# Kernel optimization log

Hardware: AMD Instinct MI355X
Metric: run time of the kernel (lower is better)

## Reference

```python
import jax, jax.numpy as jnp
import numpy as np

B, N, H, D = 16, 512, 8, 128  # batch, nodes, heads, hid_dim (per-head dim == hid_dim)


def setup_inputs() -> dict:
    key = jax.random.key(0)
    ks = jax.random.split(key, 12)
    x = jax.random.normal(ks[0], (B, N, D), dtype=jnp.float32)
    dist = jax.random.normal(ks[1], (B, N, N), dtype=jnp.float32)
    mask = (jax.random.uniform(ks[2], (B, N)) < 0.9).astype(jnp.float32)
    w_std = 0.02
    Wq = jax.random.normal(ks[3], (D, H * D), dtype=jnp.float32) * w_std
    Wk = jax.random.normal(ks[4], (D, H * D), dtype=jnp.float32) * w_std
    Wv = jax.random.normal(ks[5], (D, H * D), dtype=jnp.float32) * w_std
    Wo = jax.random.normal(ks[6], (H * D, D), dtype=jnp.float32) * w_std
    bq = jax.random.normal(ks[7], (H * D,), dtype=jnp.float32) * w_std
    bk = jax.random.normal(ks[8], (H * D,), dtype=jnp.float32) * w_std
    bv = jax.random.normal(ks[9], (H * D,), dtype=jnp.float32) * w_std
    bo = jax.random.normal(ks[10], (D,), dtype=jnp.float32) * w_std
    return {"x": x, "dist": dist, "mask": mask,
            "Wq": Wq, "bq": bq, "Wk": Wk, "bk": bk,
            "Wv": Wv, "bv": bv, "Wo": Wo, "bo": bo}


def reference(x, dist, mask, Wq, bq, Wk, bk, Wv, bv, Wo, bo):
    scale = jnp.asarray(D, x.dtype) ** -0.5
    # projections: [B,N,H*D] -> [B,H,N,D]
    q = (x @ Wq + bq).reshape(B, N, H, D).transpose(0, 2, 1, 3)
    k = (x @ Wk + bk).reshape(B, N, H, D).transpose(0, 2, 1, 3)
    v = (x @ Wv + bv).reshape(B, N, H, D).transpose(0, 2, 1, 3)
    m = mask[:, None, :, None]  # [B,1,N,1]
    q = q * m * scale
    k = k * m
    v = v * m
    a = jnp.einsum('bhnd,bhmd->bhnm', q, k)  # [B,H,N,N]
    a = a + dist[:, None, :, :]  # dist bias broadcast over heads
    amask = (mask[:, :, None] * mask[:, None, :])[:, None, :, :]  # [B,1,N,N]
    a = jnp.where(amask == 0, jnp.asarray(-1e9, a.dtype), a)
    a = jax.nn.softmax(a, axis=-1)
    a = jnp.where(amask == 0, jnp.asarray(0.0, a.dtype), a)
    y = jnp.einsum('bhnm,bhmd->bhnd', a, v)
    y = y.transpose(0, 2, 1, 3).reshape(B, N, H * D)
    y = y @ Wo + bo
    return y * mask[:, :, None]
```

## Files before the change

### kernel.cpp

```cpp
#include <hip/hip_runtime.h>
#include <hip/hip_bf16.h>

#define B_ 16
#define N_ 512
#define H_ 8
#define D_ 128
#define HD_ 1024
#define SCALE_ 0.08838834764831845f

typedef __attribute__((ext_vector_type(8))) short bf16x8;
typedef __attribute__((ext_vector_type(4))) float f32x4;
typedef __attribute__((ext_vector_type(4))) _Float16 f16x4;

__device__ __forceinline__ unsigned short f2bf(float f) {
    union { __hip_bfloat16 h; unsigned short u; } cv;
    cv.h = __float2bfloat16(f);
    return cv.u;
}
__device__ __forceinline__ unsigned short f2h(float f) {
    union { _Float16 h; unsigned short u; } cv;
    cv.h = (_Float16)f;
    return cv.u;
}

__global__ __launch_bounds__(256) void prep_kernel(
    const float* __restrict__ Wq, const float* __restrict__ Wk,
    const float* __restrict__ Wv, const float* __restrict__ Wo,
    unsigned short* __restrict__ wTh, unsigned short* __restrict__ woT)
{
    __shared__ float T[32][33];
    const int tile = blockIdx.x;
    const int t = threadIdx.x;
    if (tile < 384) {
        const int w = tile / 128;
        const int rem = tile % 128;
        const int kt = rem & 3;
        const int ct = rem >> 2;
        const float* W = (w == 0) ? Wq : (w == 1) ? Wk : Wv;
        const int k0 = kt * 32, c0 = ct * 32;
        #pragma unroll
        for (int u = 0; u < 4; u++) {
            int lin = t + 256 * u; int r = lin >> 5, c = lin & 31;
            T[r][c] = W[(size_t)(k0 + r) * 1024 + c0 + c];
        }
        __syncthreads();
        unsigned short* oh = wTh + (size_t)w * 131072;
        #pragma unroll
        for (int u = 0; u < 4; u++) {
            int lin = t + 256 * u; int c = lin >> 5, r = lin & 31;
            oh[(size_t)(c0 + c) * 128 + k0 + r] = f2bf(T[r][c]);
        }
    } else {
        const int rem = tile - 384;
        const int nt = rem & 3;
        const int kt = rem >> 2;
        const int k0 = kt * 32, n0 = nt * 32;
        #pragma unroll
        for (int u = 0; u < 4; u++) {
            int lin = t + 256 * u; int r = lin >> 5, c = lin & 31;
            T[r][c] = Wo[(size_t)(k0 + r) * 128 + n0 + c];
        }
        __syncthreads();
        #pragma unroll
        for (int u = 0; u < 4; u++) {
            int lin = t + 256 * u; int c = lin >> 5, r = lin & 31;
            woT[(size_t)(n0 + c) * 1024 + k0 + r] = f2bf(T[r][c]);
        }
    }
}

__global__ __launch_bounds__(256, 3) void qkv_kernel(
    const float* __restrict__ x, const float* __restrict__ mask,
    const unsigned short* __restrict__ wTh,
    const float* __restrict__ bq, const float* __restrict__ bk,
    const float* __restrict__ bv,
    unsigned short* __restrict__ q, unsigned short* __restrict__ k,
    unsigned short* __restrict__ vT)
{
    const int cb = blockIdx.x % 24;
    const int by = blockIdx.x / 24;
    const int row0 = by * 128, c0 = cb * 128;
    const int which = c0 >> 10, w0 = c0 & 1023;
    const float* bi = (which == 0) ? bq : (which == 1) ? bk : bv;

    __shared__ alignas(16) unsigned short Wh[128][136];
    __shared__ float biS[128];
    __shared__ float mskS[128];

    const int t = threadIdx.x;
    if (t < 128) { biS[t] = bi[w0 + t]; mskS[t] = mask[row0 + t]; }

    const unsigned short* whp = wTh + (size_t)which * 131072 + (size_t)w0 * 128;
    #pragma unroll
    for (int u = 0; u < 8; u++) {
        int lin = t + 256 * u; int c = lin >> 4, k8 = (lin & 15) * 8;
        *(bf16x8*)&Wh[c][k8] = *(const bf16x8*)&whp[(size_t)c * 128 + k8];
    }

    const int wave = t >> 6, lane = t & 63, m16 = lane & 15, g4 = lane >> 4;
    const int rw = row0 + wave * 32;

    bf16x8 ah[2][4];
    #pragma unroll
    for (int mt = 0; mt < 2; mt++)
        #pragma unroll
        for (int kc = 0; kc < 4; kc++) {
            const float* xp = &x[(size_t)(rw + mt * 16 + m16) * 128 + kc * 32 + g4 * 8];
            float4 v0 = *(const float4*)xp;
            float4 v1 = *(const float4*)(xp + 4);
            float vv[8] = {v0.x, v0.y, v0.z, v0.w, v1.x, v1.y, v1.z, v1.w};
            union { bf16x8 v; unsigned short s[8]; } Hh;
            #pragma unroll
            for (int e = 0; e < 8; e++) Hh.s[e] = f2bf(vv[e]);
            ah[mt][kc] = Hh.v;
        }
    __syncthreads();

    const f32x4 zero = {0.f, 0.f, 0.f, 0.f};
    f32x4 acc[2][8];
    #pragma unroll
    for (int mt = 0; mt < 2; mt++)
        #pragma unroll
        for (int nt = 0; nt < 8; nt++) acc[mt][nt] = zero;

    #pragma unroll
    for (int nt = 0; nt < 8; nt++) {
        #pragma unroll
        for (int kc = 0; kc < 4; kc++) {
            bf16x8 bh = *(const bf16x8*)&Wh[nt * 16 + m16][kc * 32 + g4 * 8];
            #pragma unroll
            for (int mt = 0; mt < 2; mt++)
                acc[mt][nt] = __builtin_amdgcn_mfma_f32_16x16x32_bf16(ah[mt][kc], bh, acc[mt][nt], 0, 0, 0);
        }
    }
    __syncthreads();

    const int b = row0 >> 9, h = w0 >> 7;
    const int iseq0 = row0 & 511;
    unsigned short* Tr = &Wh[0][0];

    if (which == 2) {
        #pragma unroll
        for (int mt = 0; mt < 2; mt++)
            #pragma unroll
            for (int nt = 0; nt < 8; nt++)
                #pragma unroll
                for (int r = 0; r < 4; r++) {
                    int rowl = wave * 32 + mt * 16 + g4 * 4 + r;
                    int col = nt * 16 + m16;
                    Tr[col * 136 + rowl] = f2h((acc[mt][nt][r] + biS[col]) * mskS[rowl]);
                }
        __syncthreads();
        unsigned short* vbase = vT + (size_t)(b * 8 + h) * 128 * 512 + iseq0;
        #pragma unroll
        for (int u = 0; u < 8; u++) {
            int lin = t + 256 * u; int dl = lin >> 4, i8 = (lin & 15) * 8;
            *(bf16x8*)&vbase[(size_t)dl * 512 + i8] = *(const bf16x8*)&Tr[dl * 136 + i8];
        }
    } else {
        const float sc = (which == 0) ? SCALE_ : 1.0f;
        #pragma unroll
        for (int mt = 0; mt < 2; mt++)
            #pragma unroll
            for (int nt = 0; nt < 8; nt++)
                #pragma unroll
                for (int r = 0; r < 4; r++) {
                    int rowl = wave * 32 + mt * 16 + g4 * 4 + r;
                    int col = nt * 16 + m16;
                    Tr[rowl * 136 + col] = f2bf((acc[mt][nt][r] + biS[col]) * (mskS[rowl] * sc));
                }
        __syncthreads();
        unsigned short* dst = ((which == 0) ? q : k) +
                              ((size_t)(b * 8 + h) * 512 + iseq0) * 128;
        #pragma unroll
        for (int u = 0; u < 8; u++) {
            int lin = t + 256 * u; int rl = lin >> 4, c8 = (lin & 15) * 8;
            *(bf16x8*)&dst[(size_t)rl * 128 + c8] = *(const bf16x8*)&Tr[rl * 136 + c8];
        }
    }
}

__global__ __launch_bounds__(256, 3) void attn_kernel(
    const unsigned short* __restrict__ q, const unsigned short* __restrict__ k,
    const unsigned short* __restrict__ vT, const float* __restrict__ dist,
    const float* __restrict__ mask, unsigned short* __restrict__ y)
{
    const int xid = blockIdx.x;
    const int bh = (xid & 7) | ((xid >> 6) << 3);
    const int itile = (xid >> 3) & 7;
    const int b = bh >> 3, h = bh & 7;
    const int i0 = itile * 64;

    const unsigned short* qb = q + (size_t)bh * 512 * 128;
    const unsigned short* kb = k + (size_t)bh * 512 * 128;
    const unsigned short* vb = vT + (size_t)bh * 128 * 512;

    __shared__ alignas(16) unsigned short Ks[64][136];
    __shared__ alignas(16) unsigned short Vs[128][76];
    __shared__ alignas(16) float cmS[512];

    const int t = threadIdx.x;
    const int wave = t >> 6, lane = t & 63;
    const int m16 = lane & 15, g4 = lane >> 4;
    const int iw = i0 + wave * 16;

    cmS[t] = (mask[b * 512 + t] == 0.0f) ? -1e9f : 0.0f;
    cmS[256 + t] = (mask[b * 512 + 256 + t] == 0.0f) ? -1e9f : 0.0f;

    bf16x8 aq[4];
    #pragma unroll
    for (int c = 0; c < 4; c++)
        aq[c] = *(const bf16x8*)(qb + (size_t)(iw + m16) * 128 + c * 32 + g4 * 8);

    const int krow = t >> 2, kcol = (t & 3) * 32;
    const int vrow = t >> 1, vcol = (t & 1) * 32;

    const float* dbase = dist + ((size_t)b * 512 + iw) * 512;

    float4 dvA[4];
    {
        bf16x8 kp[4], vp[4];
        #pragma unroll
        for (int u = 0; u < 4; u++) {
            kp[u] = *(const bf16x8*)(kb + (size_t)krow * 128 + kcol + u * 8);
            vp[u] = *(const bf16x8*)(vb + (size_t)vrow * 512 + vcol + u * 8);
        }
        #pragma unroll
        for (int jt = 0; jt < 4; jt++)
            dvA[jt] = *(const float4*)&dbase[(size_t)m16 * 512 + jt * 16 + g4 * 4];
        #pragma unroll
        for (int u = 0; u < 4; u++) {
            *(bf16x8*)&Ks[krow][kcol + u * 8] = kp[u];
            union { bf16x8 v8; ushort4 h4[2]; } cv; cv.v8 = vp[u];
            *(ushort4*)&Vs[vrow][vcol + u * 8] = cv.h4[0];
            *(ushort4*)&Vs[vrow][vcol + u * 8 + 4] = cv.h4[1];
        }
    }
    __syncthreads();

    const f32x4 zero = {0.f, 0.f, 0.f, 0.f};
    float rm = -3.0e38f, rl = 0.f;
    f32x4 Ot[8] = {zero, zero, zero, zero, zero, zero, zero, zero};

    for (int c = 0; c < 8; c++) {
        const int j0 = c * 64;
        bf16x8 kp[4], vp[4];
        float4 dvB[4];
        if (c < 7) {
            const int j0n = j0 + 64;
            #pragma unroll
            for (int u = 0; u < 4; u++) {
                kp[u] = *(const bf16x8*)(kb + (size_t)(j0n + krow) * 128 + kcol + u * 8);
                vp[u] = *(const bf16x8*)(vb + (size_t)vrow * 512 + j0n + vcol + u * 8);
            }
            #pragma unroll
            for (int jt = 0; jt < 4; jt++)
                dvB[jt] = *(const float4*)&dbase[(size_t)m16 * 512 + j0n + jt * 16 + g4 * 4];
        }

        f32x4 s[4];
        #pragma unroll
        for (int jt = 0; jt < 4; jt++) {
            float4 cm4 = *(const float4*)&cmS[j0 + jt * 16 + g4 * 4];
            f32x4 a = {dvA[jt].x + cm4.x, dvA[jt].y + cm4.y,
                       dvA[jt].z + cm4.z, dvA[jt].w + cm4.w};
            #pragma unroll
            for (int cc = 0; cc < 4; cc++) {
                bf16x8 kf = *(const bf16x8*)&Ks[jt * 16 + m16][cc * 32 + g4 * 8];
                a = __builtin_amdgcn_mfma_f32_16x16x32_bf16(kf, aq[cc], a, 0, 0, 0);
            }
            s[jt] = a;
        }

        float cm = -3.0e38f;
        #pragma unroll
        for (int jt = 0; jt < 4; jt++)
            #pragma unroll
            for (int r = 0; r < 4; r++) cm = fmaxf(cm, s[jt][r]);
        cm = fmaxf(cm, __shfl_xor(cm, 16));
        cm = fmaxf(cm, __shfl_xor(cm, 32));

        float nm = fmaxf(rm, cm);
        float alpha = __expf(rm - nm);
        rm = nm;
        rl *= alpha;

        f16x4 pa[4];
        float ps = 0.f;
        #pragma unroll
        for (int jt = 0; jt < 4; jt++) {
            #pragma unroll
            for (int r = 0; r < 4; r++) {
                float p = __expf(s[jt][r] - rm);
                ps += p;
                pa[jt][r] = (_Float16)p;
            }
        }
        ps += __shfl_xor(ps, 16);
        ps += __shfl_xor(ps, 32);
        rl += ps;

        float a4[4];
        #pragma unroll
        for (int r = 0; r < 4; r++) a4[r] = __shfl(alpha, g4 * 4 + r);
        #pragma unroll
        for (int dt = 0; dt < 8; dt++)
            #pragma unroll
            for (int r = 0; r < 4; r++) Ot[dt][r] *= a4[r];

        #pragma unroll
        for (int jt = 0; jt < 4; jt++)
            #pragma unroll
            for (int dt = 0; dt < 8; dt++) {
                f16x4 vf = *(const f16x4*)&Vs[dt * 16 + m16][jt * 16 + g4 * 4];
                Ot[dt] = __builtin_amdgcn_mfma_f32_16x16x16f16(pa[jt], vf, Ot[dt], 0, 0, 0);
            }

        if (c < 7) {
            __syncthreads();
            #pragma unroll
            for (int u = 0; u < 4; u++) {
                *(bf16x8*)&Ks[krow][kcol + u * 8] = kp[u];
                union { bf16x8 v8; ushort4 h4[2]; } cv; cv.v8 = vp[u];
                *(ushort4*)&Vs[vrow][vcol + u * 8] = cv.h4[0];
                *(ushort4*)&Vs[vrow][vcol + u * 8 + 4] = cv.h4[1];
            }
            #pragma unroll
            for (int jt = 0; jt < 4; jt++) dvA[jt] = dvB[jt];
            __syncthreads();
        }
    }

    __syncthreads();
    float rs = (rl > 0.f) ? 1.0f / rl : 0.f;
    float rs4[4];
    #pragma unroll
    for (int r = 0; r < 4; r++) rs4[r] = __shfl(rs, g4 * 4 + r);
    #pragma unroll
    for (int dt = 0; dt < 8; dt++)
        #pragma unroll
        for (int r = 0; r < 4; r++)
            Ks[wave * 16 + g4 * 4 + r][dt * 16 + m16] = f2bf(Ot[dt][r] * rs4[r]);
    #pragma unroll
    for (int u = 0; u < 4; u++) {
        int lin = lane + 64 * u;
        int row = lin >> 4, seg = lin & 15;
        *(bf16x8*)&y[((size_t)(b * 512) + iw + row) * 1024 + h * 128 + seg * 8] =
            *(const bf16x8*)&Ks[wave * 16 + row][seg * 8];
    }
}

__global__ __launch_bounds__(256, 2) void oproj_kernel(
    const unsigned short* __restrict__ Y, const unsigned short* __restrict__ woT,
    const float* __restrict__ bo, const float* __restrict__ mask,
    float* __restrict__ out)
{
    const int row0 = blockIdx.x * 16;
    __shared__ alignas(16) unsigned short Ys[16][136];
    __shared__ alignas(16) unsigned short Ws[128][136];
    __shared__ float boS[128];
    __shared__ float mskS[16];

    const int t = threadIdx.x;
    if (t < 128) boS[t] = bo[t];
    if (t < 16) mskS[t] = mask[row0 + t];

    const int wave = t >> 6, lane = t & 63;
    const int m16 = lane & 15, g4 = lane >> 4;
    const int n0 = wave * 32;

    const int yr = t >> 4, yk = (t & 15) * 8;
    const int wn = t >> 4, wk = (t & 15) * 8;

    const f32x4 zero = {0.f, 0.f, 0.f, 0.f};
    f32x4 acc[2] = {zero, zero};

    bf16x8 yp, wp[8];
    yp = *(const bf16x8*)&Y[(size_t)(row0 + yr) * 1024 + yk];
    #pragma unroll
    for (int u = 0; u < 8; u++)
        wp[u] = *(const bf16x8*)&woT[(size_t)(wn + u * 16) * 1024 + wk];

    for (int c = 0; c < 8; c++) {
        __syncthreads();
        *(bf16x8*)&Ys[yr][yk] = yp;
        #pragma unroll
        for (int u = 0; u < 8; u++) *(bf16x8*)&Ws[wn + u * 16][wk] = wp[u];
        __syncthreads();
        if (c < 7) {
            const int kc0 = (c + 1) * 128;
            yp = *(const bf16x8*)&Y[(size_t)(row0 + yr) * 1024 + kc0 + yk];
            #pragma unroll
            for (int u = 0; u < 8; u++)
                wp[u] = *(const bf16x8*)&woT[(size_t)(wn + u * 16) * 1024 + kc0 + wk];
        }
        #pragma unroll
        for (int kc = 0; kc < 4; kc++) {
            bf16x8 a = *(const bf16x8*)&Ys[m16][kc * 32 + g4 * 8];
            #pragma unroll
            for (int nt = 0; nt < 2; nt++) {
                bf16x8 bb = *(const bf16x8*)&Ws[n0 + nt * 16 + m16][kc * 32 + g4 * 8];
                acc[nt] = __builtin_amdgcn_mfma_f32_16x16x32_bf16(a, bb, acc[nt], 0, 0, 0);
            }
        }
    }
    __syncthreads();

    float* Ot = (float*)&Ws[0][0];
    #pragma unroll
    for (int nt = 0; nt < 2; nt++)
        #pragma unroll
        for (int r = 0; r < 4; r++) {
            int rowl = g4 * 4 + r;
            int col = n0 + nt * 16 + m16;
            Ot[rowl * 132 + col] = (acc[nt][r] + boS[col]) * mskS[rowl];
        }
    __syncthreads();
    #pragma unroll
    for (int u = 0; u < 2; u++) {
        int lin = t + 256 * u; int r = lin >> 5, c4 = lin & 31;
        *(float4*)&out[(size_t)(row0 + r) * 128 + c4 * 4] =
            *(const float4*)&Ot[r * 132 + c4 * 4];
    }
}

extern "C" void kernel_launch(void* const* d_in, const int* in_sizes, int n_in,
                              void* d_out, int out_size, void* d_ws, size_t ws_size,
                              hipStream_t stream) {
    const float* x    = (const float*)d_in[0];
    const float* dist = (const float*)d_in[1];
    const float* mask = (const float*)d_in[2];
    const float* Wq   = (const float*)d_in[3];
    const float* bq   = (const float*)d_in[4];
    const float* Wk   = (const float*)d_in[5];
    const float* bk   = (const float*)d_in[6];
    const float* Wv   = (const float*)d_in[7];
    const float* bv   = (const float*)d_in[8];
    const float* Wo   = (const float*)d_in[9];
    const float* bo   = (const float*)d_in[10];
    float* out = (float*)d_out;

    const size_t per = (size_t)B_ * H_ * N_ * D_;
    unsigned short* qb  = (unsigned short*)d_ws;
    unsigned short* kb  = qb + per;
    unsigned short* vb  = kb + per;
    unsigned short* yb  = vb + per;
    unsigned short* wTh = yb + per;
    unsigned short* woT = wTh + 3 * 131072;

    prep_kernel<<<512, 256, 0, stream>>>(Wq, Wk, Wv, Wo, wTh, woT);
    qkv_kernel<<<1536, 256, 0, stream>>>(x, mask, wTh, bq, bk, bv, qb, kb, vb);
    attn_kernel<<<1024, 256, 0, stream>>>(qb, kb, vb, dist, mask, yb);
    oproj_kernel<<<512, 256, 0, stream>>>(yb, woT, bo, mask, out);
}
```

Baseline: 161.6 us.

## Double-buffer K/V tiles in LDS with two-deep register prefetch in attention

The attention kernel now keeps two shared-memory buffers for the K and V tiles. It holds register prefetches for the next two 64-key chunks and unrolls the loop in pairs through a macro. Each chunk writes the following tile into the alternate buffer while computing on the current one, so it needs one barrier per chunk instead of two. This hides global-load latency and cuts synchronisation, at the cost of about twice the LDS and more registers. Launch bounds drop from 3 to 2 blocks per CU to fit that.

Result: no change. 162.8 us (+0.7%).

```diff
diff --git a/kernel.cpp b/kernel.cpp
--- a/kernel.cpp
+++ b/kernel.cpp
@@ -180,7 +180,91 @@
     }
 }
 
-__global__ __launch_bounds__(256, 3) void attn_kernel(
+#define ATTN_CHUNK(J0, BSEL, kpC, vpC, dvC, kpO, vpO, DO_LOAD, DO_WRITE, DO_BAR) \
+  {                                                                           \
+    const int j0_ = (J0);                                                     \
+                                     \
+    f32x4 s_[4];                                                              \
+    _Pragma("unroll")                                                         \
+    for (int jt = 0; jt < 4; jt++) {                                          \
+      float4 cm4 = *(const float4*)&cmS[j0_ + jt * 16 + g4 * 4];              \
+      f32x4 a = {dvC[jt].x + cm4.x, dvC[jt].y + cm4.y,                        \
+                 dvC[jt].z + cm4.z, dvC[jt].w + cm4.w};                       \
+      _Pragma("unroll")                                                       \
+      for (int cc = 0; cc < 4; cc++) {                                        \
+        bf16x8 kf = *(const bf16x8*)&Ks[BSEL][jt * 16 + m16][cc * 32 + g4 * 8];\
+        a = __builtin_amdgcn_mfma_f32_16x16x32_bf16(kf, aq[cc], a, 0, 0, 0);  \
+      }                                                                       \
+      s_[jt] = a;                                                             \
+    }                                                                         \
+               \
+    if (DO_LOAD) {                                                            \
+      const int j0n_ = j0_ + 128;                                             \
+      _Pragma("unroll")                                                       \
+      for (int u = 0; u < 4; u++) {                                           \
+        kpC[u] = *(const bf16x8*)(kb + (size_t)(j0n_ + krow) * 128 + kcol + u * 8); \
+        vpC[u] = *(const bf16x8*)(vb + (size_t)vrow * 512 + j0n_ + vcol + u * 8);   \
+      }                                                                       \
+      _Pragma("unroll")                                                       \
+      for (int jt = 0; jt < 4; jt++)                                          \
+        dvC[jt] = *(const float4*)&dbase[(size_t)m16 * 512 + j0n_ + jt * 16 + g4 * 4]; \
+    }                                                                         \
+                                                                 \
+    float cmax_ = -3.0e38f;                                                   \
+    _Pragma("unroll")                                                         \
+    for (int jt = 0; jt < 4; jt++)                                            \
+      _Pragma("unroll")                                                       \
+      for (int r = 0; r < 4; r++) cmax_ = fmaxf(cmax_, s_[jt][r]);            \
+    cmax_ = fmaxf(cmax_, __shfl_xor(cmax_, 16));                              \
+    cmax_ = fmaxf(cmax_, __shfl_xor(cmax_, 32));                              \
+    float nm_ = fmaxf(rm, cmax_);                                             \
+    float alpha_ = __expf(rm - nm_);                                          \
+    rm = nm_;                                                                 \
+    rl *= alpha_;                                                             \
+    f16x4 pa_[4];                                                             \
+    float ps_ = 0.f;                                                          \
+    _Pragma("unroll")                                                         \
+    for (int jt = 0; jt < 4; jt++) {                                          \
+      _Pragma("unroll")                                                       \
+      for (int r = 0; r < 4; r++) {                                           \
+        float p = __expf(s_[jt][r] - rm);                                     \
+        ps_ += p;                                                             \
+        pa_[jt][r] = (_Float16)p;                                             \
+      }                                                                       \
+    }                                                                         \
+    ps_ += __shfl_xor(ps_, 16);                                               \
+    ps_ += __shfl_xor(ps_, 32);                                               \
+    rl += ps_;                                                                \
+    float a4_[4];                                                             \
+    _Pragma("unroll")                                                         \
+    for (int r = 0; r < 4; r++) a4_[r] = __shfl(alpha_, g4 * 4 + r);          \
+    _Pragma("unroll")                                                         \
+    for (int dt = 0; dt < 8; dt++)                                            \
+      _Pragma("unroll")                                                       \
+      for (int r = 0; r < 4; r++) Ot[dt][r] *= a4_[r];                        \
+               \
+    if (DO_WRITE) {                                                           \
+      const int bo_ = (BSEL) ^ 1;                                             \
+      _Pragma("unroll")                                                       \
+      for (int u = 0; u < 4; u++) {                                           \
+        *(bf16x8*)&Ks[bo_][krow][kcol + u * 8] = kpO[u];                      \
+        union { bf16x8 v8; ushort4 h4[2]; } cv_; cv_.v8 = vpO[u];             \
+        *(ushort4*)&Vs[bo_][vrow][vcol + u * 8] = cv_.h4[0];                  \
+        *(ushort4*)&Vs[bo_][vrow][vcol + u * 8 + 4] = cv_.h4[1];              \
+      }                                                                       \
+    }                                                                         \
+                                                                      \
+    _Pragma("unroll")                                                         \
+    for (int jt = 0; jt < 4; jt++)                                            \
+      _Pragma("unroll")                                                       \
+      for (int dt = 0; dt < 8; dt++) {                                        \
+        f16x4 vf = *(const f16x4*)&Vs[BSEL][dt * 16 + m16][jt * 16 + g4 * 4]; \
+        Ot[dt] = __builtin_amdgcn_mfma_f32_16x16x16f16(pa_[jt], vf, Ot[dt], 0, 0, 0); \
+      }                                                                       \
+    if (DO_BAR) __syncthreads();                                              \
+  }
+
+__global__ __launch_bounds__(256, 2) void attn_kernel(
     const unsigned short* __restrict__ q, const unsigned short* __restrict__ k,
     const unsigned short* __restrict__ vT, const float* __restrict__ dist,
     const float* __restrict__ mask, unsigned short* __restrict__ y)
@@ -195,8 +279,8 @@
     const unsigned short* kb = k + (size_t)bh * 512 * 128;
     const unsigned short* vb = vT + (size_t)bh * 128 * 512;
 
-    __shared__ alignas(16) unsigned short Ks[64][136];
-    __shared__ alignas(16) unsigned short Vs[128][76];
+    __shared__ alignas(16) unsigned short Ks[2][64][136];
+    __shared__ alignas(16) unsigned short Vs[2][128][76];
     __shared__ alignas(16) float cmS[512];
 
     const int t = threadIdx.x;
@@ -217,24 +301,30 @@
 
     const float* dbase = dist + ((size_t)b * 512 + iw) * 512;
 
-    float4 dvA[4];
-    {
-        bf16x8 kp[4], vp[4];
-        #pragma unroll
-        for (int u = 0; u < 4; u++) {
-            kp[u] = *(const bf16x8*)(kb + (size_t)krow * 128 + kcol + u * 8);
-            vp[u] = *(const bf16x8*)(vb + (size_t)vrow * 512 + vcol + u * 8);
-        }
-        #pragma unroll
-        for (int jt = 0; jt < 4; jt++)
-            dvA[jt] = *(const float4*)&dbase[(size_t)m16 * 512 + jt * 16 + g4 * 4];
-        #pragma unroll
-        for (int u = 0; u < 4; u++) {
-            *(bf16x8*)&Ks[krow][kcol + u * 8] = kp[u];
-            union { bf16x8 v8; ushort4 h4[2]; } cv; cv.v8 = vp[u];
-            *(ushort4*)&Vs[vrow][vcol + u * 8] = cv.h4[0];
-            *(ushort4*)&Vs[vrow][vcol + u * 8 + 4] = cv.h4[1];
-        }
+    bf16x8 kpA[4], vpA[4], kpB[4], vpB[4];
+    float4 dvA[4], dvB[4];
+    #pragma unroll
+    for (int u = 0; u < 4; u++) {
+        kpA[u] = *(const bf16x8*)(kb + (size_t)krow * 128 + kcol + u * 8);
+        vpA[u] = *(const bf16x8*)(vb + (size_t)vrow * 512 + vcol + u * 8);
+    }
+    #pragma unroll
+    for (int jt = 0; jt < 4; jt++)
+        dvA[jt] = *(const float4*)&dbase[(size_t)m16 * 512 + jt * 16 + g4 * 4];
+    #pragma unroll
+    for (int u = 0; u < 4; u++) {
+        kpB[u] = *(const bf16x8*)(kb + (size_t)(64 + krow) * 128 + kcol + u * 8);
+        vpB[u] = *(const bf16x8*)(vb + (size_t)vrow * 512 + 64 + vcol + u * 8);
+    }
+    #pragma unroll
+    for (int jt = 0; jt < 4; jt++)
+        dvB[jt] = *(const float4*)&dbase[(size_t)m16 * 512 + 64 + jt * 16 + g4 * 4];
+    #pragma unroll
+    for (int u = 0; u < 4; u++) {
+        *(bf16x8*)&Ks[0][krow][kcol + u * 8] = kpA[u];
+        union { bf16x8 v8; ushort4 h4[2]; } cv; cv.v8 = vpA[u];
+        *(ushort4*)&Vs[0][vrow][vcol + u * 8] = cv.h4[0];
+        *(ushort4*)&Vs[0][vrow][vcol + u * 8 + 4] = cv.h4[1];
     }
     __syncthreads();
 
@@ -242,96 +332,14 @@
     float rm = -3.0e38f, rl = 0.f;
     f32x4 Ot[8] = {zero, zero, zero, zero, zero, zero, zero, zero};
 
-    for (int c = 0; c < 8; c++) {
-        const int j0 = c * 64;
-        bf16x8 kp[4], vp[4];
-        float4 dvB[4];
-        if (c < 7) {
-            const int j0n = j0 + 64;
-            #pragma unroll
-            for (int u = 0; u < 4; u++) {
-                kp[u] = *(const bf16x8*)(kb + (size_t)(j0n + krow) * 128 + kcol + u * 8);
-                vp[u] = *(const bf16x8*)(vb + (size_t)vrow * 512 + j0n + vcol + u * 8);
-            }
-            #pragma unroll
-            for (int jt = 0; jt < 4; jt++)
-                dvB[jt] = *(const float4*)&dbase[(size_t)m16 * 512 + j0n + jt * 16 + g4 * 4];
-        }
-
-        f32x4 s[4];
-        #pragma unroll
-        for (int jt = 0; jt < 4; jt++) {
-            float4 cm4 = *(const float4*)&cmS[j0 + jt * 16 + g4 * 4];
-            f32x4 a = {dvA[jt].x + cm4.x, dvA[jt].y + cm4.y,
-                       dvA[jt].z + cm4.z, dvA[jt].w + cm4.w};
-            #pragma unroll
-            for (int cc = 0; cc < 4; cc++) {
-                bf16x8 kf = *(const bf16x8*)&Ks[jt * 16 + m16][cc * 32 + g4 * 8];
-                a = __builtin_amdgcn_mfma_f32_16x16x32_bf16(kf, aq[cc], a, 0, 0, 0);
-            }
-            s[jt] = a;
-        }
-
-        float cm = -3.0e38f;
-        #pragma unroll
-        for (int jt = 0; jt < 4; jt++)
-            #pragma unroll
-            for (int r = 0; r < 4; r++) cm = fmaxf(cm, s[jt][r]);
-        cm = fmaxf(cm, __shfl_xor(cm, 16));
-        cm = fmaxf(cm, __shfl_xor(cm, 32));
-
-        float nm = fmaxf(rm, cm);
-        float alpha = __expf(rm - nm);
-        rm = nm;
-        rl *= alpha;
-
-        f16x4 pa[4];
-        float ps = 0.f;
-        #pragma unroll
-        for (int jt = 0; jt < 4; jt++) {
-            #pragma unroll
-            for (int r = 0; r < 4; r++) {
-                float p = __expf(s[jt][r] - rm);
-                ps += p;
-                pa[jt][r] = (_Float16)p;
-            }
-        }
-        ps += __shfl_xor(ps, 16);
-        ps += __shfl_xor(ps, 32);
-        rl += ps;
-
-        float a4[4];
-        #pragma unroll
-        for (int r = 0; r < 4; r++) a4[r] = __shfl(alpha, g4 * 4 + r);
-        #pragma unroll
-        for (int dt = 0; dt < 8; dt++)
-            #pragma unroll
-            for (int r = 0; r < 4; r++) Ot[dt][r] *= a4[r];
-
-        #pragma unroll
-        for (int jt = 0; jt < 4; jt++)
-            #pragma unroll
-            for (int dt = 0; dt < 8; dt++) {
-                f16x4 vf = *(const f16x4*)&Vs[dt * 16 + m16][jt * 16 + g4 * 4];
-                Ot[dt] = __builtin_amdgcn_mfma_f32_16x16x16f16(pa[jt], vf, Ot[dt], 0, 0, 0);
-            }
-
-        if (c < 7) {
-            __syncthreads();
-            #pragma unroll
-            for (int u = 0; u < 4; u++) {
-                *(bf16x8*)&Ks[krow][kcol + u * 8] = kp[u];
-                union { bf16x8 v8; ushort4 h4[2]; } cv; cv.v8 = vp[u];
-                *(ushort4*)&Vs[vrow][vcol + u * 8] = cv.h4[0];
-                *(ushort4*)&Vs[vrow][vcol + u * 8 + 4] = cv.h4[1];
-            }
-            #pragma unroll
-            for (int jt = 0; jt < 4; jt++) dvA[jt] = dvB[jt];
-            __syncthreads();
-        }
-    }
-
-    __syncthreads();
+    for (int c2 = 0; c2 < 3; c2++) {
+        const int j0p = c2 * 128;
+        ATTN_CHUNK(j0p,      0, kpA, vpA, dvA, kpB, vpB, 1, 1, 1)
+        ATTN_CHUNK(j0p + 64, 1, kpB, vpB, dvB, kpA, vpA, 1, 1, 1)
+    }
+    ATTN_CHUNK(384, 0, kpA, vpA, dvA, kpB, vpB, 0, 1, 1)
+    ATTN_CHUNK(448, 1, kpB, vpB, dvB, kpA, vpA, 0, 0, 0)
+
     float rs = (rl > 0.f) ? 1.0f / rl : 0.f;
     float rs4[4];
     #pragma unroll
@@ -340,13 +348,13 @@
     for (int dt = 0; dt < 8; dt++)
         #pragma unroll
         for (int r = 0; r < 4; r++)
-            Ks[wave * 16 + g4 * 4 + r][dt * 16 + m16] = f2bf(Ot[dt][r] * rs4[r]);
+            Ks[0][wave * 16 + g4 * 4 + r][dt * 16 + m16] = f2bf(Ot[dt][r] * rs4[r]);
     #pragma unroll
     for (int u = 0; u < 4; u++) {
         int lin = lane + 64 * u;
         int row = lin >> 4, seg = lin & 15;
         *(bf16x8*)&y[((size_t)(b * 512) + iw + row) * 1024 + h * 128 + seg * 8] =
-            *(const bf16x8*)&Ks[wave * 16 + row][seg * 8];
+            *(const bf16x8*)&Ks[0][wave * 16 + row][seg * 8];
     }
 }
 
```
